# Performance work log

Measured on AMD Instinct MI355X. Metric: run time of the kernel, lower is better.

## Reference

```python
import jax, jax.numpy as jnp
from jax import lax
import numpy as np

GAMMA, ALPHA, BETA, THETA = 0.5, 0.5, 1.0, 1.0
BLOCK = 512  # tile size over the p2 point dim for the streaming K=1 knn


def _min_sqdist(p1, p2):
    """K=1 knn_points: min squared distance from each p1 point to p2. (B,N1,3),(B,N2,3) -> (B,N1).
    Streams p2 in blocks with a running min, never materializing the full NxM matrix."""
    B, N2, _ = p2.shape
    nb = N2 // BLOCK
    p2b = jnp.transpose(p2.reshape(B, nb, BLOCK, 3), (1, 0, 2, 3))  # (nb,B,BLOCK,3)
    p1sq = jnp.sum(p1 * p1, axis=-1)  # (B,N1)

    def step(carry, chunk):
        # ||a-b||^2 = ||a||^2 - 2 a.b + ||b||^2
        d = (p1sq[:, :, None]
             - 2.0 * jnp.einsum('bnd,bmd->bnm', p1, chunk)
             + jnp.sum(chunk * chunk, axis=-1)[:, None, :])
        return jnp.minimum(carry, jnp.min(d, axis=-1)), None

    init = jnp.full(p1sq.shape, jnp.inf, dtype=p1.dtype)
    out, _ = lax.scan(step, init, p2b)
    return out


def _pnt2quat(grasp_pred):
    center = grasp_pred[..., :3]
    q = grasp_pred[..., 3:]
    q = q / jnp.sqrt(jnp.sum(q * q, axis=-1, keepdims=True) + 1e-12)
    return center, q


def _mat2quat(g):
    R = g[..., :3, :3]
    t = g[..., :3, 3]
    tr = R[..., 0, 0] + R[..., 1, 1] + R[..., 2, 2]
    w = 0.5 * jnp.sqrt(jnp.maximum(1.0 + tr, 1e-12))
    inv4w = 1.0 / (4.0 * w)
    x = (R[..., 2, 1] - R[..., 1, 2]) * inv4w
    y = (R[..., 0, 2] - R[..., 2, 0]) * inv4w
    z = (R[..., 1, 0] - R[..., 0, 1]) * inv4w
    q = jnp.stack([w, x, y, z], axis=-1)
    return t, q


def setup_inputs() -> dict:
    key = jax.random.key(0)
    ks = jax.random.split(key, 8)
    B, N, M = 4, 16384, 2048
    xyz = jax.random.normal(ks[0], (B, N, 3), dtype=jnp.float32)
    sample_xyz = jax.random.normal(ks[1], (B, M, 3), dtype=jnp.float32)
    temp = jnp.asarray(0.5, dtype=jnp.float32)
    grasp_pred = jax.random.normal(ks[2], (B, M, 7), dtype=jnp.float32)
    # build valid SE(3) ground-truth grasps: rotation from unit quaternion (w>=0) + translation
    q = jax.random.normal(ks[3], (B, M, 4), dtype=jnp.float32)
    q = q / jnp.sqrt(jnp.sum(q * q, axis=-1, keepdims=True) + 1e-12)
    q = jnp.where(q[..., :1] < 0, -q, q)
    w, x, y, z = q[..., 0], q[..., 1], q[..., 2], q[..., 3]
    R = jnp.stack([
        jnp.stack([1 - 2 * (y * y + z * z), 2 * (x * y - w * z), 2 * (x * z + w * y)], -1),
        jnp.stack([2 * (x * y + w * z), 1 - 2 * (x * x + z * z), 2 * (y * z - w * x)], -1),
        jnp.stack([2 * (x * z - w * y), 2 * (y * z + w * x), 1 - 2 * (x * x + y * y)], -1),
    ], -2)  # (B,M,3,3)
    t = jax.random.normal(ks[4], (B, M, 3), dtype=jnp.float32)
    top = jnp.concatenate([R, t[..., None]], axis=-1)  # (B,M,3,4)
    bottom = jnp.broadcast_to(jnp.array([0., 0., 0., 1.], jnp.float32), (B, M, 1, 4))
    grasp_gt = jnp.concatenate([top, bottom], axis=-2)  # (B,M,4,4)
    class_pred = jax.random.uniform(ks[5], (B, M), dtype=jnp.float32, minval=1e-4, maxval=1.0 - 1e-4)
    class_gt = (jax.random.uniform(ks[6], (B, M)) < 0.5).astype(jnp.float32)
    return {"xyz": xyz, "sample_xyz": sample_xyz, "temp": temp, "grasp_pred": grasp_pred,
            "grasp_gt": grasp_gt, "class_pred": class_pred, "class_gt": class_gt}


def reference(xyz, sample_xyz, temp, grasp_pred, grasp_gt, class_pred, class_gt):
    # sample loss (chamfer-style with K=1 knn in both directions + max-min coverage term)
    d_smp_org = _min_sqdist(sample_xyz, xyz)   # (B,M)
    d_org_smp = _min_sqdist(xyz, sample_xyz)   # (B,N)
    sample_loss = (jnp.mean(d_smp_org)
                   + jnp.mean(jnp.max(d_smp_org, axis=-1))
                   + GAMMA * jnp.mean(d_org_smp))
    # projection loss
    proj_loss = temp ** 2
    center_pred, quat_pred = _pnt2quat(grasp_pred)
    center_gt, quat_gt = _mat2quat(grasp_gt)
    cls_w = class_gt.reshape(-1)
    dist = jnp.linalg.norm(center_pred.reshape(-1, 3) - center_gt.reshape(-1, 3) + 1e-6, axis=-1)
    trans_loss = jnp.mean(dist * cls_w)
    dot = jnp.sum(quat_pred.reshape(-1, 4) * quat_gt.reshape(-1, 4), axis=-1)
    rot = jnp.arccos(jnp.clip(jnp.abs(dot), 0.0, 1.0 - 1e-7))
    rot_loss = jnp.mean(rot * cls_w)
    reg_loss = trans_loss + ALPHA * rot_loss
    # classification loss (BCE on probabilities)
    p = jnp.clip(class_pred, 1e-7, 1.0 - 1e-7)
    cls_loss = -jnp.mean(class_gt * jnp.log(p) + (1.0 - class_gt) * jnp.log(1.0 - p))
    return THETA * sample_loss + proj_loss + BETA * reg_loss + cls_loss
```

## Files before the change

kernel.cpp:

```cpp
#include <hip/hip_runtime.h>
#include <math.h>

#define BB 4
#define NN 16384
#define MM 2048
#define BM (BB*MM)
#define BN (BB*NN)

#define TGT 1024
#define QPB 512
#define S1  16
#define S2  2

#define PART1OFF 0
#define PART2OFF (S1*BM)
#define REDOFF   (PART1OFF + S1*BM + S2*BN)
#define R_SUMS1  (REDOFF)
#define R_MAXES  (REDOFF+8)
#define R_SUMS2  (REDOFF+16)
#define R_GST    (REDOFF+80)
#define R_GSR    (REDOFF+112)
#define R_GSC    (REDOFF+144)

__global__ __launch_bounds__(256) void k_min(const float* __restrict__ xyz,
                                             const float* __restrict__ smp,
                                             float* __restrict__ ws) {
    __shared__ float4 tgt[TGT];
    const int tid = threadIdx.x;
    const int bx  = blockIdx.x;
    const float* qptr; const float* tptr; float* outp;
    if (bx < 256) {
        int qb = bx >> 1, s = bx & 1;
        int gq = qb * QPB;
        int b  = gq >> 14;
        qptr = xyz + (size_t)gq * 3;
        tptr = smp + (size_t)(b * MM + s * TGT) * 3;
        outp = ws + PART2OFF + s * BN + gq;
    } else {
        int bx2 = bx - 256;
        int qb = bx2 >> 4, s = bx2 & 15;
        int gq = qb * QPB;
        int b  = gq >> 11;
        qptr = smp + (size_t)gq * 3;
        tptr = xyz + (size_t)(b * NN + s * TGT) * 3;
        outp = ws + PART1OFF + s * BM + gq;
    }
    for (int p = tid; p < TGT; p += 256) {
        float x = tptr[3*p], y = tptr[3*p+1], z = tptr[3*p+2];
        tgt[p] = make_float4(-2.0f*x, -2.0f*y, -2.0f*z, x*x + y*y + z*z);
    }
    float qx0 = qptr[3*tid],       qy0 = qptr[3*tid+1],       qz0 = qptr[3*tid+2];
    float qx1 = qptr[3*(tid+256)], qy1 = qptr[3*(tid+256)+1], qz1 = qptr[3*(tid+256)+2];
    float mn0 = INFINITY, mn1 = INFINITY;
    __syncthreads();
#pragma unroll 4
    for (int j = 0; j < TGT; j += 2) {
        float4 ta = tgt[j], tb = tgt[j+1];
        float d0a = fmaf(ta.x, qx0, fmaf(ta.y, qy0, fmaf(ta.z, qz0, ta.w)));
        float d0b = fmaf(tb.x, qx0, fmaf(tb.y, qy0, fmaf(tb.z, qz0, tb.w)));
        mn0 = fminf(mn0, fminf(d0a, d0b));
        float d1a = fmaf(ta.x, qx1, fmaf(ta.y, qy1, fmaf(ta.z, qz1, ta.w)));
        float d1b = fmaf(tb.x, qx1, fmaf(tb.y, qy1, fmaf(tb.z, qz1, tb.w)));
        mn1 = fminf(mn1, fminf(d1a, d1b));
    }
    outp[tid]       = mn0 + (qx0*qx0 + qy0*qy0 + qz0*qz0);
    outp[tid + 256] = mn1 + (qx1*qx1 + qy1*qy1 + qz1*qz1);
}

__device__ __forceinline__ float blockSum256(float v, volatile float* s4) {
#pragma unroll
    for (int o = 32; o > 0; o >>= 1) v += __shfl_down(v, o, 64);
    __syncthreads();
    int lane = threadIdx.x & 63, w = threadIdx.x >> 6;
    if (lane == 0) s4[w] = v;
    __syncthreads();
    return s4[0] + s4[1] + s4[2] + s4[3];
}

__device__ __forceinline__ float blockMax256(float v, volatile float* s4) {
#pragma unroll
    for (int o = 32; o > 0; o >>= 1) v = fmaxf(v, __shfl_down(v, o, 64));
    __syncthreads();
    int lane = threadIdx.x & 63, w = threadIdx.x >> 6;
    if (lane == 0) s4[w] = v;
    __syncthreads();
    return fmaxf(fmaxf(s4[0], s4[1]), fmaxf(s4[2], s4[3]));
}

__global__ __launch_bounds__(256) void k_reduce(const float* __restrict__ gp,
                                                const float* __restrict__ gg,
                                                const float* __restrict__ cp,
                                                const float* __restrict__ cg,
                                                float* __restrict__ ws) {
    __shared__ float s4a[4], s4b[4], s4c[4];
    const int bx = blockIdx.x, tid = threadIdx.x;
    if (bx < 8) {
        float s = 0.0f, mx = -INFINITY;
#pragma unroll
        for (int k = 0; k < 4; ++k) {
            int q = bx * 1024 + tid + k * 256;
            float v = INFINITY;
#pragma unroll
            for (int sp = 0; sp < S1; ++sp) v = fminf(v, ws[PART1OFF + sp * BM + q]);
            s += v; mx = fmaxf(mx, v);
        }
        float bs = blockSum256(s, s4a);
        float bm = blockMax256(mx, s4b);
        if (tid == 0) { ws[R_SUMS1 + bx] = bs; ws[R_MAXES + bx] = bm; }
    } else if (bx < 72) {
        int i = bx - 8;
        float s = 0.0f;
#pragma unroll
        for (int k = 0; k < 4; ++k) {
            int q = i * 1024 + tid + k * 256;
            s += fminf(ws[PART2OFF + q], ws[PART2OFF + BN + q]);
        }
        float bs = blockSum256(s, s4a);
        if (tid == 0) ws[R_SUMS2 + i] = bs;
    } else {
        int m = (bx - 72) * 256 + tid;
        const float* g = gp + (size_t)m * 7;
        float cxp = g[0], cyp = g[1], czp = g[2];
        float q0 = g[3], q1 = g[4], q2 = g[5], q3 = g[6];
        float invq = 1.0f / sqrtf(q0*q0 + q1*q1 + q2*q2 + q3*q3 + 1e-12f);
        const float* G = gg + (size_t)m * 16;
        float tr = G[0] + G[5] + G[10];
        float w = 0.5f * sqrtf(fmaxf(1.0f + tr, 1e-12f));
        float inv4w = 1.0f / (4.0f * w);
        float gqx = (G[9] - G[6]) * inv4w;
        float gqy = (G[2] - G[8]) * inv4w;
        float gqz = (G[4] - G[1]) * inv4w;
        float cw = cg[m];
        float dx = cxp - G[3]  + 1e-6f;
        float dy = cyp - G[7]  + 1e-6f;
        float dz = czp - G[11] + 1e-6f;
        float dist = sqrtf(dx*dx + dy*dy + dz*dz);
        float dot = (q0*w + q1*gqx + q2*gqy + q3*gqz) * invq;
        float rot = acosf(fminf(fabsf(dot), 1.0f - 1e-7f));
        float p = fminf(fmaxf(cp[m], 1e-7f), 1.0f - 1e-7f);
        float ce = cw * logf(p) + (1.0f - cw) * logf(1.0f - p);
        float s1 = blockSum256(dist * cw, s4a);
        float s2 = blockSum256(rot  * cw, s4b);
        float s3 = blockSum256(ce, s4c);
        int i = bx - 72;
        if (tid == 0) { ws[R_GST + i] = s1; ws[R_GSR + i] = s2; ws[R_GSC + i] = s3; }
    }
}

__global__ __launch_bounds__(256) void k_final(const float* __restrict__ temp,
                                               const float* __restrict__ ws,
                                               float* __restrict__ out) {
    __shared__ float s4[4];
    const int tid = threadIdx.x;
    float a = (tid < 8)  ? ws[R_SUMS1 + tid] : 0.0f;
    float f = (tid < 4)  ? fmaxf(ws[R_MAXES + 2*tid], ws[R_MAXES + 2*tid + 1]) : 0.0f;
    float b = (tid < 64) ? ws[R_SUMS2 + tid] : 0.0f;
    float c = (tid < 32) ? ws[R_GST + tid] : 0.0f;
    float d = (tid < 32) ? ws[R_GSR + tid] : 0.0f;
    float e = (tid < 32) ? ws[R_GSC + tid] : 0.0f;
    float A = blockSum256(a, s4);
    float F = blockSum256(f, s4);
    float B = blockSum256(b, s4);
    float C = blockSum256(c, s4);
    float D = blockSum256(d, s4);
    float E = blockSum256(e, s4);
    if (tid == 0) {
        float sample = A * (1.0f / BM) + F * 0.25f + 0.5f * B * (1.0f / BN);
        float reg    = C * (1.0f / BM) + 0.5f * D * (1.0f / BM);
        float cls    = -E * (1.0f / BM);
        float t = temp[0];
        out[0] = sample + t * t + reg + cls;
    }
}

extern "C" void kernel_launch(void* const* d_in, const int* in_sizes, int n_in,
                              void* d_out, int out_size, void* d_ws, size_t ws_size,
                              hipStream_t stream) {
    const float* xyz  = (const float*)d_in[0];
    const float* smp  = (const float*)d_in[1];
    const float* temp = (const float*)d_in[2];
    const float* gp   = (const float*)d_in[3];
    const float* gg   = (const float*)d_in[4];
    const float* cp   = (const float*)d_in[5];
    const float* cg   = (const float*)d_in[6];
    float* ws  = (float*)d_ws;
    float* out = (float*)d_out;

    hipLaunchKernelGGL(k_min,    dim3(512), dim3(256), 0, stream, xyz, smp, ws);
    hipLaunchKernelGGL(k_reduce, dim3(104), dim3(256), 0, stream, gp, gg, cp, cg, ws);
    hipLaunchKernelGGL(k_final,  dim3(1),   dim3(256), 0, stream, temp, ws, out);
}
```

Before: 98.31 us.

## Register-block 8 queries per thread and shrink target tiles in knn min kernel

Result: faster. 96.33 us (-2.0%).

```diff
diff --git a/kernel.cpp b/kernel.cpp
--- a/kernel.cpp
+++ b/kernel.cpp
@@ -7,20 +7,19 @@
 #define BM (BB*MM)
 #define BN (BB*NN)
 
-#define TGT 1024
-#define QPB 512
-#define S1  16
-#define S2  2
+#define TGT 256
+#define S1  64
+#define S2  8
 
 #define PART1OFF 0
 #define PART2OFF (S1*BM)
 #define REDOFF   (PART1OFF + S1*BM + S2*BN)
 #define R_SUMS1  (REDOFF)
-#define R_MAXES  (REDOFF+8)
-#define R_SUMS2  (REDOFF+16)
-#define R_GST    (REDOFF+80)
-#define R_GSR    (REDOFF+112)
-#define R_GSC    (REDOFF+144)
+#define R_MAXES  (REDOFF+32)
+#define R_SUMS2  (REDOFF+64)
+#define R_GST    (REDOFF+128)
+#define R_GSR    (REDOFF+160)
+#define R_GSC    (REDOFF+192)
 
 __global__ __launch_bounds__(256) void k_min(const float* __restrict__ xyz,
                                              const float* __restrict__ smp,
@@ -30,41 +29,46 @@
     const int bx  = blockIdx.x;
     const float* qptr; const float* tptr; float* outp;
     if (bx < 256) {
-        int qb = bx >> 1, s = bx & 1;
-        int gq = qb * QPB;
-        int b  = gq >> 14;
+        int b = bx >> 6, r = bx & 63, qb = r >> 3, s = r & 7;
+        int gq = b * NN + qb * 2048;
         qptr = xyz + (size_t)gq * 3;
         tptr = smp + (size_t)(b * MM + s * TGT) * 3;
         outp = ws + PART2OFF + s * BN + gq;
     } else {
         int bx2 = bx - 256;
-        int qb = bx2 >> 4, s = bx2 & 15;
-        int gq = qb * QPB;
-        int b  = gq >> 11;
+        int b = bx2 >> 6, s = bx2 & 63;
+        int gq = b * MM;
         qptr = smp + (size_t)gq * 3;
         tptr = xyz + (size_t)(b * NN + s * TGT) * 3;
         outp = ws + PART1OFF + s * BM + gq;
     }
-    for (int p = tid; p < TGT; p += 256) {
-        float x = tptr[3*p], y = tptr[3*p+1], z = tptr[3*p+2];
-        tgt[p] = make_float4(-2.0f*x, -2.0f*y, -2.0f*z, x*x + y*y + z*z);
+    {
+        float x = tptr[3*tid], y = tptr[3*tid+1], z = tptr[3*tid+2];
+        tgt[tid] = make_float4(-2.0f*x, -2.0f*y, -2.0f*z, x*x + y*y + z*z);
     }
-    float qx0 = qptr[3*tid],       qy0 = qptr[3*tid+1],       qz0 = qptr[3*tid+2];
-    float qx1 = qptr[3*(tid+256)], qy1 = qptr[3*(tid+256)+1], qz1 = qptr[3*(tid+256)+2];
-    float mn0 = INFINITY, mn1 = INFINITY;
+    float qx[8], qy[8], qz[8], mn[8];
+#pragma unroll
+    for (int k = 0; k < 8; ++k) {
+        int q = tid + k * 256;
+        qx[k] = qptr[3*q]; qy[k] = qptr[3*q+1]; qz[k] = qptr[3*q+2];
+        mn[k] = INFINITY;
+    }
     __syncthreads();
-#pragma unroll 4
+#pragma unroll 2
     for (int j = 0; j < TGT; j += 2) {
         float4 ta = tgt[j], tb = tgt[j+1];
-        float d0a = fmaf(ta.x, qx0, fmaf(ta.y, qy0, fmaf(ta.z, qz0, ta.w)));
-        float d0b = fmaf(tb.x, qx0, fmaf(tb.y, qy0, fmaf(tb.z, qz0, tb.w)));
-        mn0 = fminf(mn0, fminf(d0a, d0b));
-        float d1a = fmaf(ta.x, qx1, fmaf(ta.y, qy1, fmaf(ta.z, qz1, ta.w)));
-        float d1b = fmaf(tb.x, qx1, fmaf(tb.y, qy1, fmaf(tb.z, qz1, tb.w)));
-        mn1 = fminf(mn1, fminf(d1a, d1b));
+#pragma unroll
+        for (int k = 0; k < 8; ++k) {
+            float da = fmaf(ta.x, qx[k], fmaf(ta.y, qy[k], fmaf(ta.z, qz[k], ta.w)));
+            float db = fmaf(tb.x, qx[k], fmaf(tb.y, qy[k], fmaf(tb.z, qz[k], tb.w)));
+            mn[k] = fminf(mn[k], fminf(da, db));
+        }
     }
-    outp[tid]       = mn0 + (qx0*qx0 + qy0*qy0 + qz0*qz0);
-    outp[tid + 256] = mn1 + (qx1*qx1 + qy1*qy1 + qz1*qz1);
+#pragma unroll
+    for (int k = 0; k < 8; ++k) {
+        int q = tid + k * 256;
+        outp[q] = mn[k] + (qx[k]*qx[k] + qy[k]*qy[k] + qz[k]*qz[k]);
+    }
 }
 
 __device__ __forceinline__ float blockSum256(float v, volatile float* s4) {
@@ -94,31 +98,29 @@
                                                 float* __restrict__ ws) {
     __shared__ float s4a[4], s4b[4], s4c[4];
     const int bx = blockIdx.x, tid = threadIdx.x;
-    if (bx < 8) {
-        float s = 0.0f, mx = -INFINITY;
+    if (bx < 32) {
+        int q = bx * 256 + tid;
+        float v = INFINITY;
 #pragma unroll
-        for (int k = 0; k < 4; ++k) {
-            int q = bx * 1024 + tid + k * 256;
-            float v = INFINITY;
-#pragma unroll
-            for (int sp = 0; sp < S1; ++sp) v = fminf(v, ws[PART1OFF + sp * BM + q]);
-            s += v; mx = fmaxf(mx, v);
-        }
-        float bs = blockSum256(s, s4a);
-        float bm = blockMax256(mx, s4b);
+        for (int sp = 0; sp < S1; ++sp) v = fminf(v, ws[PART1OFF + sp * BM + q]);
+        float bs = blockSum256(v, s4a);
+        float bm = blockMax256(v, s4b);
         if (tid == 0) { ws[R_SUMS1 + bx] = bs; ws[R_MAXES + bx] = bm; }
-    } else if (bx < 72) {
-        int i = bx - 8;
+    } else if (bx < 96) {
+        int i = bx - 32;
         float s = 0.0f;
 #pragma unroll
         for (int k = 0; k < 4; ++k) {
             int q = i * 1024 + tid + k * 256;
-            s += fminf(ws[PART2OFF + q], ws[PART2OFF + BN + q]);
+            float v = INFINITY;
+#pragma unroll
+            for (int sp = 0; sp < S2; ++sp) v = fminf(v, ws[PART2OFF + sp * BN + q]);
+            s += v;
         }
         float bs = blockSum256(s, s4a);
         if (tid == 0) ws[R_SUMS2 + i] = bs;
     } else {
-        int m = (bx - 72) * 256 + tid;
+        int m = (bx - 96) * 256 + tid;
         const float* g = gp + (size_t)m * 7;
         float cxp = g[0], cyp = g[1], czp = g[2];
         float q0 = g[3], q1 = g[4], q2 = g[5], q3 = g[6];
@@ -142,7 +144,7 @@
         float s1 = blockSum256(dist * cw, s4a);
         float s2 = blockSum256(rot  * cw, s4b);
         float s3 = blockSum256(ce, s4c);
-        int i = bx - 72;
+        int i = bx - 96;
         if (tid == 0) { ws[R_GST + i] = s1; ws[R_GSR + i] = s2; ws[R_GSC + i] = s3; }
     }
 }
@@ -152,8 +154,13 @@
                                                float* __restrict__ out) {
     __shared__ float s4[4];
     const int tid = threadIdx.x;
-    float a = (tid < 8)  ? ws[R_SUMS1 + tid] : 0.0f;
-    float f = (tid < 4)  ? fmaxf(ws[R_MAXES + 2*tid], ws[R_MAXES + 2*tid + 1]) : 0.0f;
+    float a = (tid < 32) ? ws[R_SUMS1 + tid] : 0.0f;
+    float f = 0.0f;
+    if (tid < 4) {
+        f = -INFINITY;
+#pragma unroll
+        for (int r = 0; r < 8; ++r) f = fmaxf(f, ws[R_MAXES + tid * 8 + r]);
+    }
     float b = (tid < 64) ? ws[R_SUMS2 + tid] : 0.0f;
     float c = (tid < 32) ? ws[R_GST + tid] : 0.0f;
     float d = (tid < 32) ? ws[R_GSR + tid] : 0.0f;
@@ -187,6 +194,6 @@
     float* out = (float*)d_out;
 
     hipLaunchKernelGGL(k_min,    dim3(512), dim3(256), 0, stream, xyz, smp, ws);
-    hipLaunchKernelGGL(k_reduce, dim3(104), dim3(256), 0, stream, gp, gg, cp, cg, ws);
+    hipLaunchKernelGGL(k_reduce, dim3(128), dim3(256), 0, stream, gp, gg, cp, cg, ws);
     hipLaunchKernelGGL(k_final,  dim3(1),   dim3(256), 0, stream, temp, ws, out);
 }
```
